# Kernel tuning notes

Measured on AMD Instinct MI355X. Metric: run time of the kernel, lower is better.

## Reference

```python
import jax, jax.numpy as jnp
import numpy as np

NUM_HEADS = 16
D_K = 8  # == n_qubits


def setup_inputs() -> dict:
    key = jax.random.key(0)
    k1, k2, k3 = jax.random.split(key, 3)
    x = jax.random.normal(k1, (4, 2048, 128), dtype=jnp.float32)
    # trainable RX angles, one per qubit (tq.RX has_params=True)
    theta = jax.random.normal(k2, (D_K,), dtype=jnp.float32)
    # out_proj: Linear(embed_dim, embed_dim, bias=False)
    w_out = jax.random.normal(k3, (128, 128), dtype=jnp.float32) * (1.0 / np.sqrt(128.0))
    return {"x": x, "theta": theta, "w_out": w_out}


def quantum_features(x, theta):
    # x: [b, s, e]. Per head of size d_k: encode RX(x_i), trainable RX(theta_i)
    # (composes to RX(x_i + theta_i)), CNOT ladder [i, i+1], measure PauliZ.
    # Heisenberg picture: Z_w -> Z_0...Z_w, so <Z_w> = prod_{i<=w} cos(x_i + theta_i).
    b, s, e = x.shape
    heads = x.reshape(b, s, NUM_HEADS, D_K)
    return jnp.cumprod(jnp.cos(heads + theta), axis=-1)  # [b, s, h, d_k]


def reference(x, theta, w_out):
    b, s, e = x.shape
    # q == k == v: same shared q_layer applied to the same x three times.
    qkv = quantum_features(x, theta)            # [b, s, h, d_k]
    q = qkv.transpose(0, 2, 1, 3)               # [b, h, s, d_k]
    scores = jnp.einsum('bhqd,bhkd->bhqk', q, q) / np.sqrt(D_K)
    attn = jax.nn.softmax(scores, axis=-1)      # dropout is identity at eval
    out = jnp.einsum('bhqk,bhkd->bhqd', attn, q)
    out = out.transpose(0, 2, 1, 3).reshape(b, s, e)
    return out @ w_out.T
```

## Files before the change

### kernel.cpp

```cpp
#include <hip/hip_runtime.h>

#define BATCH 4
#define SEQ   2048
#define EMB   128
#define NH    16
#define DK    8

#define QSCALE 0.510069726f

typedef _Float16 v4h  __attribute__((ext_vector_type(4)));
typedef _Float16 v8h  __attribute__((ext_vector_type(8)));
typedef __fp16   v2fp __attribute__((ext_vector_type(2)));
typedef float    v4f  __attribute__((ext_vector_type(4)));
typedef float    v16f __attribute__((ext_vector_type(16)));

#define CHUNK  512
#define NCH    (SEQ / CHUNK)
#define VTP    520

__launch_bounds__(256, 4)
__global__ void attn_kernel(const float* __restrict__ x,
                            const float* __restrict__ theta,
                            _Float16* __restrict__ Ah ) {
  __shared__ __align__(16) _Float16 Kl[CHUNK * 8];
  __shared__ __align__(16) _Float16 VT[10][VTP];

  const int tid = threadIdx.x;
  const int L   = tid & 63;
  const int ln  = L & 31;
  const int hf  = L >> 5;
  const int wv  = tid >> 6;
  const int bh     = blockIdx.x >> 4;
  const int qchunk = blockIdx.x & 15;
  const int qb     = qchunk * 128 + wv * 32;
  const int b = bh >> 4;
  const int h = bh & 15;

  float th[DK];
#pragma unroll
  for (int i = 0; i < DK; ++i) th[i] = theta[i];

  for (int i = tid; i < VTP; i += 256) {
    VT[8][i] = (_Float16)1.0f;
    VT[9][i] = (_Float16)0.0f;
  }

  const int c0 = qchunk >> 2;
  const int mrow = (ln < 9) ? ln : 9;
  const float* xb = x + (size_t)b * SEQ * EMB + h * DK;

  float4 pa0, pa1, pb0, pb1;
  {
    const float* xp = xb + (size_t)(c0 * CHUNK + tid) * EMB;
    pa0 = *(const float4*)(xp);
    pa1 = *(const float4*)(xp + 4);
    pb0 = *(const float4*)(xp + 256 * EMB);
    pb1 = *(const float4*)(xp + 256 * EMB + 4);
  }

  v8h qf = {0, 0, 0, 0, 0, 0, 0, 0};
  v16f acc;
#pragma unroll
  for (int i = 0; i < 16; ++i) acc[i] = 0.f;
  v16f zf;
#pragma unroll
  for (int i = 0; i < 16; ++i) zf[i] = 0.f;

  for (int cc = 0; cc < NCH; ++cc) {
    if (cc) __syncthreads();

    {
      float r0[8], r1[8];
      r0[0] = __cosf(pa0.x + th[0]);
      r0[1] = r0[0] * __cosf(pa0.y + th[1]);
      r0[2] = r0[1] * __cosf(pa0.z + th[2]);
      r0[3] = r0[2] * __cosf(pa0.w + th[3]);
      r0[4] = r0[3] * __cosf(pa1.x + th[4]);
      r0[5] = r0[4] * __cosf(pa1.y + th[5]);
      r0[6] = r0[5] * __cosf(pa1.z + th[6]);
      r0[7] = r0[6] * __cosf(pa1.w + th[7]);
      r1[0] = __cosf(pb0.x + th[0]);
      r1[1] = r1[0] * __cosf(pb0.y + th[1]);
      r1[2] = r1[1] * __cosf(pb0.z + th[2]);
      r1[3] = r1[2] * __cosf(pb0.w + th[3]);
      r1[4] = r1[3] * __cosf(pb1.x + th[4]);
      r1[5] = r1[4] * __cosf(pb1.y + th[5]);
      r1[6] = r1[5] * __cosf(pb1.z + th[6]);
      r1[7] = r1[6] * __cosf(pb1.w + th[7]);

      _Float16 h0[8], h1[8];
#pragma unroll
      for (int i = 0; i < 8; ++i) { h0[i] = (_Float16)r0[i]; h1[i] = (_Float16)r1[i]; }

      union { v4h v[2]; float4 f; } u0, u1;
      u0.v[0] = (v4h){h0[0], h0[1], h0[2], h0[3]};
      u0.v[1] = (v4h){h0[4], h0[5], h0[6], h0[7]};
      u1.v[0] = (v4h){h1[0], h1[1], h1[2], h1[3]};
      u1.v[1] = (v4h){h1[4], h1[5], h1[6], h1[7]};
      *(float4*)&Kl[tid * 8]         = u0.f;
      *(float4*)&Kl[(tid + 256) * 8] = u1.f;

      const int j0 = tid, j1 = tid + 256;
      const int col0 = (j0 & ~15) | (j0 & 3) | ((j0 & 4) << 1) | ((j0 & 8) >> 1);
      const int col1 = (j1 & ~15) | (j1 & 3) | ((j1 & 4) << 1) | ((j1 & 8) >> 1);
#pragma unroll
      for (int d = 0; d < 8; ++d) {
        VT[d][col0] = h0[d];
        VT[d][col1] = h1[d];
      }
    }
    __syncthreads();

    if (cc + 1 < NCH) {
      const int cn = (c0 + cc + 1) & (NCH - 1);
      const float* xp = xb + (size_t)(cn * CHUNK + tid) * EMB;
      pa0 = *(const float4*)(xp);
      pa1 = *(const float4*)(xp + 4);
      pb0 = *(const float4*)(xp + 256 * EMB);
      pb1 = *(const float4*)(xp + 256 * EMB + 4);
    }

    if (cc == 0 && hf == 0) {
      const int ql = (qchunk & 3) * 128 + wv * 32 + ln;
      v8h qv = *(const v8h*)&Kl[ql * 8];
      const _Float16 qs = (_Float16)QSCALE;
      const v8h qsc = {qs, qs, qs, qs, qs, qs, qs, qs};
      qf = qv * qsc;
    }

    v8h kf_next = *(const v8h*)&Kl[ln * 8];
#pragma unroll 2
    for (int kb = 0; kb < CHUNK / 32; ++kb) {
      const v8h kf = kf_next;
      const v16f s = __builtin_amdgcn_mfma_f32_32x32x16_f16(kf, qf, zf, 0, 0, 0);
      if (kb + 1 < CHUNK / 32)
        kf_next = *(const v8h*)&Kl[((kb + 1) * 32 + ln) * 8];
      const v8h vt0 = *(const v8h*)&VT[mrow][kb * 32 + hf * 8];
      const v8h vt1 = *(const v8h*)&VT[mrow][kb * 32 + 16 + hf * 8];
      union { v2fp p[4]; v8h v; } p0, p1;
#pragma unroll
      for (int i = 0; i < 4; ++i) {
        p0.p[i] = __builtin_amdgcn_cvt_pkrtz(
            __builtin_amdgcn_exp2f(s[2 * i]),
            __builtin_amdgcn_exp2f(s[2 * i + 1]));
        p1.p[i] = __builtin_amdgcn_cvt_pkrtz(
            __builtin_amdgcn_exp2f(s[8 + 2 * i]),
            __builtin_amdgcn_exp2f(s[8 + 2 * i + 1]));
      }
      acc = __builtin_amdgcn_mfma_f32_32x32x16_f16(vt0, p0.v, acc, 0, 0, 0);
      acc = __builtin_amdgcn_mfma_f32_32x32x16_f16(vt1, p1.v, acc, 0, 0, 0);
    }
  }

  {
    const float den = __shfl(acc[4], ln, 64);
    const float inv = 1.0f / den;
    const int qrow = qb + ln;
    v4h o = {(_Float16)(acc[0] * inv), (_Float16)(acc[1] * inv),
             (_Float16)(acc[2] * inv), (_Float16)(acc[3] * inv)};
    *(v4h*)(Ah + ((size_t)b * SEQ + qrow) * EMB + h * DK + hf * 4) = o;
  }
}

__launch_bounds__(256, 4)
__global__ void proj_kernel(const _Float16* __restrict__ Ah,
                            const float* __restrict__ W,
                            float* __restrict__ out) {
  __shared__ __align__(16) _Float16 Ahs[64][136];
  __shared__ __align__(16) _Float16 Whs[64][136];

  const int tid  = threadIdx.x;
  const int L    = tid & 63;
  const int wv   = tid >> 6;
  const int quad = L >> 4;
  const int ln   = L & 15;
  const int rowbase = blockIdx.x * 64;
  const int colbase = blockIdx.y * 64;

#pragma unroll
  for (int it = 0; it < 4; ++it) {
    const int idx = it * 256 + tid;
    const int r  = idx >> 4;
    const int c8 = idx & 15;
    *(uint4*)&Ahs[r][c8 * 8] =
        *(const uint4*)(Ah + (size_t)(rowbase + r) * EMB + c8 * 8);
  }
#pragma unroll
  for (int it = 0; it < 8; ++it) {
    const int idx = it * 256 + tid;
    const int n  = idx >> 5;
    const int c4 = idx & 31;
    const float4 w = *(const float4*)(W + (size_t)(colbase + n) * EMB + c4 * 4);
    v4h wh = {(_Float16)w.x, (_Float16)w.y, (_Float16)w.z, (_Float16)w.w};
    *(v4h*)&Whs[n][c4 * 4] = wh;
  }
  __syncthreads();

  v4f acc[4];
#pragma unroll
  for (int nt = 0; nt < 4; ++nt) acc[nt] = (v4f){0.f, 0.f, 0.f, 0.f};

#pragma unroll
  for (int k8 = 0; k8 < 8; ++k8) {
    const v4h af = *(const v4h*)&Ahs[wv * 16 + ln][k8 * 16 + quad * 4];
#pragma unroll
    for (int nt = 0; nt < 4; ++nt) {
      const v4h bf = *(const v4h*)&Whs[nt * 16 + ln][k8 * 16 + quad * 4];
      acc[nt] = __builtin_amdgcn_mfma_f32_16x16x16f16(af, bf, acc[nt], 0, 0, 0);
    }
  }

#pragma unroll
  for (int nt = 0; nt < 4; ++nt) {
    const int col = colbase + nt * 16 + ln;
#pragma unroll
    for (int r = 0; r < 4; ++r) {
      out[(size_t)(rowbase + wv * 16 + quad * 4 + r) * EMB + col] = acc[nt][r];
    }
  }
}

extern "C" void kernel_launch(void* const* d_in, const int* in_sizes, int n_in,
                              void* d_out, int out_size, void* d_ws, size_t ws_size,
                              hipStream_t stream) {
  const float* x     = (const float*)d_in[0];
  const float* theta = (const float*)d_in[1];
  const float* w_out = (const float*)d_in[2];
  float* out = (float*)d_out;

  _Float16* Ah = (_Float16*)d_ws;

  attn_kernel<<<dim3(1024), dim3(256), 0, stream>>>(x, theta, Ah);

  proj_kernel<<<dim3((BATCH * SEQ) / 64, 2), dim3(256), 0, stream>>>(Ah, w_out, out);
}
```

Before: 93.79 us.

## Split key range across two wave groups per block and reduce partial sums

The attention block grows from 256 to 512 threads, and the four key chunks are split between two sub-groups of four waves. Each sub-group processes two chunks with its own K and VT shared buffers. Unnormalized partial accumulators, including the denominator row, are combined through shared memory before normalization. Queries are now computed directly from global x instead of from the first staged K chunk. The aim is to halve the serial per-wave loop length and raise parallelism, at the cost of double the shared memory, an extra reduction and barrier, and launch bounds of 512×8 that may constrain registers.

```diff
diff --git a/kernel.cpp b/kernel.cpp
--- a/kernel.cpp
+++ b/kernel.cpp
@@ -15,24 +15,26 @@
 typedef float    v16f __attribute__((ext_vector_type(16)));
 
 #define CHUNK  512
-#define NCH    (SEQ / CHUNK)
 #define VTP    520
 
-__launch_bounds__(256, 4)
+__launch_bounds__(512, 8)
 __global__ void attn_kernel(const float* __restrict__ x,
                             const float* __restrict__ theta,
                             _Float16* __restrict__ Ah ) {
-  __shared__ __align__(16) _Float16 Kl[CHUNK * 8];
-  __shared__ __align__(16) _Float16 VT[10][VTP];
+  __shared__ __align__(16) _Float16 Kl[2][CHUNK * 8];
+  __shared__ __align__(16) _Float16 VT[2][10][VTP];
 
   const int tid = threadIdx.x;
   const int L   = tid & 63;
   const int ln  = L & 31;
   const int hf  = L >> 5;
   const int wv  = tid >> 6;
+  const int sg  = wv >> 2;
+  const int wl  = wv & 3;
+  const int tg  = tid & 255;
   const int bh     = blockIdx.x >> 4;
   const int qchunk = blockIdx.x & 15;
-  const int qb     = qchunk * 128 + wv * 32;
+  const int qb     = qchunk * 128 + wl * 32;
   const int b = bh >> 4;
   const int h = bh & 15;
 
@@ -40,25 +42,45 @@
 #pragma unroll
   for (int i = 0; i < DK; ++i) th[i] = theta[i];
 
-  for (int i = tid; i < VTP; i += 256) {
-    VT[8][i] = (_Float16)1.0f;
-    VT[9][i] = (_Float16)0.0f;
-  }
-
-  const int c0 = qchunk >> 2;
+  for (int i = tg; i < VTP; i += 256) {
+    VT[sg][8][i] = (_Float16)1.0f;
+    VT[sg][9][i] = (_Float16)0.0f;
+  }
+
   const int mrow = (ln < 9) ? ln : 9;
   const float* xb = x + (size_t)b * SEQ * EMB + h * DK;
 
+  v8h qf = {0, 0, 0, 0, 0, 0, 0, 0};
+  if (hf == 0) {
+    const int qrow = qb + ln;
+    const float* xq = x + ((size_t)b * SEQ + qrow) * EMB + h * DK;
+    const float4 a0 = *(const float4*)(xq);
+    const float4 a1 = *(const float4*)(xq + 4);
+    float r[8];
+    r[0] = __cosf(a0.x + th[0]);
+    r[1] = r[0] * __cosf(a0.y + th[1]);
+    r[2] = r[1] * __cosf(a0.z + th[2]);
+    r[3] = r[2] * __cosf(a0.w + th[3]);
+    r[4] = r[3] * __cosf(a1.x + th[4]);
+    r[5] = r[4] * __cosf(a1.y + th[5]);
+    r[6] = r[5] * __cosf(a1.z + th[6]);
+    r[7] = r[6] * __cosf(a1.w + th[7]);
+    qf = (v8h){(_Float16)(r[0] * QSCALE), (_Float16)(r[1] * QSCALE),
+               (_Float16)(r[2] * QSCALE), (_Float16)(r[3] * QSCALE),
+               (_Float16)(r[4] * QSCALE), (_Float16)(r[5] * QSCALE),
+               (_Float16)(r[6] * QSCALE), (_Float16)(r[7] * QSCALE)};
+  }
+
+  const int cbase = sg * 2;
   float4 pa0, pa1, pb0, pb1;
   {
-    const float* xp = xb + (size_t)(c0 * CHUNK + tid) * EMB;
+    const float* xp = xb + (size_t)(cbase * CHUNK + tg) * EMB;
     pa0 = *(const float4*)(xp);
     pa1 = *(const float4*)(xp + 4);
     pb0 = *(const float4*)(xp + 256 * EMB);
     pb1 = *(const float4*)(xp + 256 * EMB + 4);
   }
 
-  v8h qf = {0, 0, 0, 0, 0, 0, 0, 0};
   v16f acc;
 #pragma unroll
   for (int i = 0; i < 16; ++i) acc[i] = 0.f;
@@ -66,8 +88,8 @@
 #pragma unroll
   for (int i = 0; i < 16; ++i) zf[i] = 0.f;
 
-  for (int cc = 0; cc < NCH; ++cc) {
-    if (cc) __syncthreads();
+  for (int cg = 0; cg < 2; ++cg) {
+    if (cg) __syncthreads();
 
     {
       float r0[8], r1[8];
@@ -97,46 +119,37 @@
       u0.v[1] = (v4h){h0[4], h0[5], h0[6], h0[7]};
       u1.v[0] = (v4h){h1[0], h1[1], h1[2], h1[3]};
       u1.v[1] = (v4h){h1[4], h1[5], h1[6], h1[7]};
-      *(float4*)&Kl[tid * 8]         = u0.f;
-      *(float4*)&Kl[(tid + 256) * 8] = u1.f;
-
-      const int j0 = tid, j1 = tid + 256;
+      *(float4*)&Kl[sg][tg * 8]         = u0.f;
+      *(float4*)&Kl[sg][(tg + 256) * 8] = u1.f;
+
+      const int j0 = tg, j1 = tg + 256;
       const int col0 = (j0 & ~15) | (j0 & 3) | ((j0 & 4) << 1) | ((j0 & 8) >> 1);
       const int col1 = (j1 & ~15) | (j1 & 3) | ((j1 & 4) << 1) | ((j1 & 8) >> 1);
 #pragma unroll
       for (int d = 0; d < 8; ++d) {
-        VT[d][col0] = h0[d];
-        VT[d][col1] = h1[d];
+        VT[sg][d][col0] = h0[d];
+        VT[sg][d][col1] = h1[d];
       }
     }
     __syncthreads();
 
-    if (cc + 1 < NCH) {
-      const int cn = (c0 + cc + 1) & (NCH - 1);
-      const float* xp = xb + (size_t)(cn * CHUNK + tid) * EMB;
+    if (cg == 0) {
+      const float* xp = xb + (size_t)((cbase + 1) * CHUNK + tg) * EMB;
       pa0 = *(const float4*)(xp);
       pa1 = *(const float4*)(xp + 4);
       pb0 = *(const float4*)(xp + 256 * EMB);
       pb1 = *(const float4*)(xp + 256 * EMB + 4);
     }
 
-    if (cc == 0 && hf == 0) {
-      const int ql = (qchunk & 3) * 128 + wv * 32 + ln;
-      v8h qv = *(const v8h*)&Kl[ql * 8];
-      const _Float16 qs = (_Float16)QSCALE;
-      const v8h qsc = {qs, qs, qs, qs, qs, qs, qs, qs};
-      qf = qv * qsc;
-    }
-
-    v8h kf_next = *(const v8h*)&Kl[ln * 8];
+    v8h kf_next = *(const v8h*)&Kl[sg][ln * 8];
 #pragma unroll 2
     for (int kb = 0; kb < CHUNK / 32; ++kb) {
       const v8h kf = kf_next;
       const v16f s = __builtin_amdgcn_mfma_f32_32x32x16_f16(kf, qf, zf, 0, 0, 0);
       if (kb + 1 < CHUNK / 32)
-        kf_next = *(const v8h*)&Kl[((kb + 1) * 32 + ln) * 8];
-      const v8h vt0 = *(const v8h*)&VT[mrow][kb * 32 + hf * 8];
-      const v8h vt1 = *(const v8h*)&VT[mrow][kb * 32 + 16 + hf * 8];
+        kf_next = *(const v8h*)&Kl[sg][((kb + 1) * 32 + ln) * 8];
+      const v8h vt0 = *(const v8h*)&VT[sg][mrow][kb * 32 + hf * 8];
+      const v8h vt1 = *(const v8h*)&VT[sg][mrow][kb * 32 + 16 + hf * 8];
       union { v2fp p[4]; v8h v; } p0, p1;
 #pragma unroll
       for (int i = 0; i < 4; ++i) {
@@ -152,7 +165,17 @@
     }
   }
 
-  {
+  __syncthreads();
+  float* part = (float*)&Kl[1][0];
+  if (sg == 1) {
+    float* p = part + (((wl * 2 + hf) * 32) + ln) * 5;
+    p[0] = acc[0]; p[1] = acc[1]; p[2] = acc[2]; p[3] = acc[3]; p[4] = acc[4];
+  }
+  __syncthreads();
+  if (sg == 0) {
+    const float* p = part + (((wl * 2 + hf) * 32) + ln) * 5;
+    acc[0] += p[0]; acc[1] += p[1]; acc[2] += p[2]; acc[3] += p[3];
+    acc[4] += p[4];
     const float den = __shfl(acc[4], ln, 64);
     const float inv = 1.0f / den;
     const int qrow = qb + ln;
@@ -230,7 +253,7 @@
 
   _Float16* Ah = (_Float16*)d_ws;
 
-  attn_kernel<<<dim3(1024), dim3(256), 0, stream>>>(x, theta, Ah);
+  attn_kernel<<<dim3(1024), dim3(512), 0, stream>>>(x, theta, Ah);
 
   proj_kernel<<<dim3((BATCH * SEQ) / 64, 2), dim3(256), 0, stream>>>(Ah, w_out, out);
 }
```

Result: slower. 101.4 us (+8.1%).
